# Kernel optimization log

Measured on AMD Instinct MI355X. Metric: run time of the kernel, lower is better.

Reference implementation:

```python
import jax, jax.numpy as jnp
import numpy as np

EMBED_DIM = 1024
EXPAND_RATIO = 128  # head_dim; n_heads = EMBED_DIM // EXPAND_RATIO = 8
B, N = 4, 2048


def setup_inputs() -> dict:
    key = jax.random.key(0)
    ks = jax.random.split(key, 6)
    std = 0.02
    d = EMBED_DIM
    return {
        "x": jax.random.normal(ks[0], (B, N, d), dtype=jnp.float32),
        "Wq": jax.random.normal(ks[1], (d, d), dtype=jnp.float32) * std,
        "Wk": jax.random.normal(ks[2], (d, d), dtype=jnp.float32) * std,
        "Wv": jax.random.normal(ks[3], (d, d), dtype=jnp.float32) * std,
        "Wo": jax.random.normal(ks[4], (d, d), dtype=jnp.float32) * std,
        "norm_w": jnp.ones((d,), dtype=jnp.float32),
    }


def _rmsnorm(x, w, eps=1e-6):
    return x * jax.lax.rsqrt(jnp.mean(x * x, axis=-1, keepdims=True) + eps) * w


def _gla_scan(q, k, v, g):
    # q,k,v,g: [b, n, h, d]; state S: [b, h, d_k, d_v]
    b, n, h, d = q.shape
    qs, ks_, vs, gs = (jnp.moveaxis(t, 1, 0) for t in (q, k, v, g))  # [n,b,h,d]
    S0 = jnp.zeros((b, h, d, d), dtype=q.dtype)

    def step(S, inp):
        q_t, k_t, v_t, g_t = inp
        # S_t = diag(exp(g_t)) S_{t-1} + k_t^T v_t (gate on key dim)
        S = jnp.exp(g_t)[..., :, None] * S + k_t[..., :, None] * v_t[..., None, :]
        o_t = jnp.einsum('bhk,bhkv->bhv', q_t, S)
        return S, o_t

    _, outs = jax.lax.scan(step, S0, (qs, ks_, vs, gs))
    return jnp.moveaxis(outs, 0, 1)  # [b, n, h, d]


def reference(x, Wq, Wk, Wv, Wo, norm_w):
    b, n, D = x.shape
    hd = EXPAND_RATIO
    h = D // hd

    q = jax.nn.silu(x @ Wq.T)          # q_activation = silu
    f = jax.nn.sigmoid(x @ Wk.T)       # f = sigmoid(k_proj(x))
    log_f = jax.nn.log_sigmoid(f)      # faithful: logsigmoid applied to f (lower_bound=None path)
    k = 1.0 - f
    v = x @ Wv.T

    def split_heads(t):
        return t.reshape(b, n, h, hd)

    out = _gla_scan(split_heads(q), split_heads(k), split_heads(v), split_heads(log_f))
    out = out.reshape(b, n, D)
    out = _rmsnorm(out, norm_w)        # norm_pos='ogate', no output gate
    return out @ Wo.T
```

## Files before the change

### kernel.cpp

```cpp
#include <hip/hip_runtime.h>
#include <cstdint>
#include <cstddef>


typedef unsigned short u16;
using f32x4  = __attribute__((ext_vector_type(4))) float;
using bf16x8 = __attribute__((ext_vector_type(8))) short;

__device__ __forceinline__ float bf2f(u16 u) {
  union { unsigned int i; float f; } v; v.i = ((unsigned int)u) << 16; return v.f;
}
__device__ __forceinline__ u16 f2bf(float f) {
  union { float f; unsigned int i; } v; v.f = f;
  unsigned int r = v.i + 0x7fffu + ((v.i >> 16) & 1u);
  return (u16)(r >> 16);
}
__device__ __forceinline__ void async_load16(const void* g, void* l) {
  __builtin_amdgcn_global_load_lds(
      (const __attribute__((address_space(1))) unsigned int*)(uintptr_t)g,
      (__attribute__((address_space(3))) unsigned int*)(uintptr_t)l, 16, 0, 0);
}

__device__ __forceinline__ void gemm128_core(const u16* __restrict__ Ag, const u16* __restrict__ Bg,
                                             u16* smem, f32x4 (&acc)[4][4]) {
  const int tid = threadIdx.x;
  const int lane = tid & 63, wave = tid >> 6;
  const int wm = (wave & 1) * 64, wn = (wave >> 1) * 64;
  const int r = lane & 15, quad = lane >> 4;
  const int xk = r & 3;
  const u16* baseA = smem + (wm + r) * 32 + ((quad ^ xk) & 3) * 8;
  const u16* baseB = smem + 4096 + (wn + r) * 32 + ((quad ^ xk) & 3) * 8;
  const int soff = (tid >> 2) * 1024 + (((tid & 3) ^ ((tid >> 2) & 3)) * 8);
  u16* dA = smem + wave * 512;
  u16* dB = smem + 4096 + wave * 512;
#pragma unroll
  for (int it = 0; it < 2; ++it) {
    async_load16(Ag + it * 65536 + soff, dA + it * 2048);
    async_load16(Bg + it * 65536 + soff, dB + it * 2048);
  }
#pragma unroll 2
  for (int kt = 0; kt < 32; ++kt) {
    const int cb = (kt & 1) * 8192;
    __syncthreads();
    if (kt < 31) {
      const int nb = ((kt + 1) & 1) * 8192;
      const u16* As = Ag + (kt + 1) * 32 + soff;
      const u16* Bs = Bg + (kt + 1) * 32 + soff;
#pragma unroll
      for (int it = 0; it < 2; ++it) {
        async_load16(As + it * 65536, dA + nb + it * 2048);
        async_load16(Bs + it * 65536, dB + nb + it * 2048);
      }
    }
    bf16x8 af[4], bv[4];
#pragma unroll
    for (int i = 0; i < 4; ++i) af[i] = *(const bf16x8*)(baseA + cb + i * 512);
#pragma unroll
    for (int j = 0; j < 4; ++j) bv[j] = *(const bf16x8*)(baseB + cb + j * 512);
#pragma unroll
    for (int i = 0; i < 4; ++i)
#pragma unroll
      for (int j = 0; j < 4; ++j)
        acc[i][j] = __builtin_amdgcn_mfma_f32_16x16x32_bf16(af[i], bv[j], acc[i][j], 0, 0, 0);
  }
}

__global__ __launch_bounds__(256) void cast_f32_bf16(const float* __restrict__ src,
                                                     u16* __restrict__ dst, int n4) {
  int i = blockIdx.x * 256 + threadIdx.x;
  if (i >= n4) return;
  float4 v = ((const float4*)src)[i];
  unsigned int lo = (unsigned)f2bf(v.x) | ((unsigned)f2bf(v.y) << 16);
  unsigned int hi = (unsigned)f2bf(v.z) | ((unsigned)f2bf(v.w) << 16);
  ((uint2*)dst)[i] = make_uint2(lo, hi);
}

__global__ __launch_bounds__(256) void cast_w4(const float* __restrict__ w0, const float* __restrict__ w1,
                                               const float* __restrict__ w2, const float* __restrict__ w3,
                                               u16* __restrict__ d0, u16* __restrict__ d1,
                                               u16* __restrict__ d2, u16* __restrict__ d3) {
  const float* src = blockIdx.y == 0 ? w0 : (blockIdx.y == 1 ? w1 : (blockIdx.y == 2 ? w2 : w3));
  u16* dst = blockIdx.y == 0 ? d0 : (blockIdx.y == 1 ? d1 : (blockIdx.y == 2 ? d2 : d3));
  int i = blockIdx.x * 256 + threadIdx.x;
  float4 v = ((const float4*)src)[i];
  unsigned int lo = (unsigned)f2bf(v.x) | ((unsigned)f2bf(v.y) << 16);
  unsigned int hi = (unsigned)f2bf(v.z) | ((unsigned)f2bf(v.w) << 16);
  ((uint2*)dst)[i] = make_uint2(lo, hi);
}

__global__ __launch_bounds__(256) void hgru_gemm_qkv(
    const u16* __restrict__ Xb, const u16* __restrict__ Wqb, const u16* __restrict__ Wkb,
    const u16* __restrict__ Wvb, u16* __restrict__ Qb, u16* __restrict__ Kb,
    u16* __restrict__ Vb) {
  __shared__ alignas(16) u16 smem[16384];
  const int which = blockIdx.y >> 3, bn = blockIdx.y & 7;
  const u16* W = which == 0 ? Wqb : (which == 1 ? Wkb : Wvb);
  const u16* Ag = Xb + (size_t)blockIdx.x * 128 * 1024;
  const u16* Bg = W + (size_t)bn * 128 * 1024;
  f32x4 acc[4][4] = {};
  gemm128_core(Ag, Bg, smem, acc);
  const int tid = threadIdx.x, lane = tid & 63, wave = tid >> 6;
  const int wm = (wave & 1) * 64, wn = (wave >> 1) * 64;
  const int r = lane & 15, quad = lane >> 4;
#pragma unroll
  for (int i = 0; i < 4; ++i)
#pragma unroll
    for (int j = 0; j < 4; ++j)
#pragma unroll
      for (int reg = 0; reg < 4; ++reg) {
        int m = blockIdx.x * 128 + wm + i * 16 + quad * 4 + reg;
        int n = bn * 128 + wn + j * 16 + r;
        size_t off = (size_t)m * 1024 + n;
        float z = acc[i][j][reg];
        if (which == 0) {
          Qb[off] = f2bf(z / (1.f + __expf(-z)));
        } else if (which == 1) {
          float ek = __expf(-z);
          Kb[off] = f2bf(ek / (1.f + ek));
        } else {
          Vb[off] = f2bf(z);
        }
      }
}

__global__ __launch_bounds__(256) void hgru_scan(
    const u16* __restrict__ Qg, const u16* __restrict__ Kg, const u16* __restrict__ Vg,
    u16* __restrict__ O) {
  __shared__ alignas(16) char smem[59008];
  float* sb = (float*)(smem);
  u16* sU   = (u16*)(smem + 16512);
  u16* sKt  = (u16*)(smem + 33920);
  u16* sVt1 = (u16*)(smem + 44160);
  u16* sQ   = (u16*)(smem + 33920);
  u16* sK   = (u16*)(smem + 42624);
  u16* sAm  = (u16*)(smem + 51328);
  u16* sVt2 = (u16*)(smem + 53888);

  const int tid = threadIdx.x, blk = blockIdx.x;
  const int vh = blk & 1, c = (blk >> 1) & 63, bh = blk >> 7, h = bh & 7, bb_ = bh >> 3;
  const size_t rb = (size_t)(bb_ * 2048 + c * 32) * 1024 + h * 128;
  const bool haveP = (c > 0);
  const size_t rb1 = haveP ? rb - 32 * 1024 : rb;

  const int lane = tid & 63, wave = tid >> 6;
  const int r = lane & 15, quad = lane >> 4;
  const int ts = tid & 31;
  const int g8 = tid >> 5;

  uint4 Q2[2], K2[2], K1[2], V2, V1;
#pragma unroll
  for (int it = 0; it < 2; ++it) {
    Q2[it] = *(const uint4*)(Qg + rb  + (size_t)ts * 1024 + (it * 8 + g8) * 8);
    K2[it] = *(const uint4*)(Kg + rb  + (size_t)ts * 1024 + (it * 8 + g8) * 8);
    K1[it] = *(const uint4*)(Kg + rb1 + (size_t)ts * 1024 + (it * 8 + g8) * 8);
  }
  V2 = *(const uint4*)(Vg + rb  + (size_t)ts * 1024 + vh * 64 + g8 * 8);
  V1 = *(const uint4*)(Vg + rb1 + (size_t)ts * 1024 + vh * 64 + g8 * 8);

  f32x4 accU[2][4] = {};
  const int vm = (wave & 1) * 32, in = (wave >> 1) * 64;

  if (haveP) {
    { const int col = tid & 127, half = tid >> 7;
      float run = 0.f;
      const size_t gb = rb1 + (size_t)(half * 16) * 1024 + col;
#pragma unroll
      for (int t = 0; t < 16; ++t) {
        float kv = bf2f(Kg[gb + (size_t)t * 1024]);
        run -= __logf(1.f + __expf(-(1.f - kv)));
        sb[(half * 16 + t) * 129 + col] = run;
      } }
    __syncthreads();
    { if (tid >> 7) { const int col = tid & 127; float fix = sb[15 * 129 + col];
#pragma unroll
        for (int t = 16; t < 32; ++t) sb[t * 129 + col] += fix; } }
    __syncthreads();
#pragma unroll
    for (int it = 0; it < 2; ++it) {
      const int i8 = it * 8 + g8;
      const u16* kp = (const u16*)&K1[it];
#pragma unroll
      for (int e = 0; e < 8; ++e) {
        int i = i8 * 8 + e;
        float bs = sb[ts * 129 + i];
        float bC = sb[31 * 129 + i];
        sKt[i * 40 + ts] = f2bf(bf2f(kp[e]) * __expf(bC - bs));
      }
    }
    { const u16* vp = (const u16*)&V1;
#pragma unroll
      for (int e = 0; e < 8; ++e) sVt1[(g8 * 8 + e) * 40 + ts] = vp[e]; }
    __syncthreads();
#pragma unroll
    for (int mi = 0; mi < 2; ++mi) {
      bf16x8 af = *(const bf16x8*)(sVt1 + (vm + mi * 16 + r) * 40 + quad * 8);
#pragma unroll
      for (int nj = 0; nj < 4; ++nj) {
        bf16x8 bv = *(const bf16x8*)(sKt + (in + nj * 16 + r) * 40 + quad * 8);
        accU[mi][nj] = __builtin_amdgcn_mfma_f32_16x16x32_bf16(af, bv, accU[mi][nj], 0, 0, 0);
      }
    }
  }
  { const int col = tid & 127, half = tid >> 7;
    float run = 0.f;
    const size_t gb = rb + (size_t)(half * 16) * 1024 + col;
#pragma unroll
    for (int t = 0; t < 16; ++t) {
      float kv = bf2f(Kg[gb + (size_t)t * 1024]);
      run -= __logf(1.f + __expf(-(1.f - kv)));
      sb[(half * 16 + t) * 129 + col] = run;
    } }
  __syncthreads();
  { if (tid >> 7) { const int col = tid & 127; float fix = sb[15 * 129 + col];
#pragma unroll
      for (int t = 16; t < 32; ++t) sb[t * 129 + col] += fix; } }
  if (haveP) {
#pragma unroll
    for (int mi = 0; mi < 2; ++mi)
#pragma unroll
      for (int nj = 0; nj < 4; ++nj)
#pragma unroll
        for (int reg = 0; reg < 4; ++reg) {
          int vl = vm + mi * 16 + quad * 4 + reg;
          int i  = in + nj * 16 + r;
          sU[vl * 136 + i] = f2bf(accU[mi][nj][reg]);
        }
  }
  __syncthreads();
#pragma unroll
  for (int it = 0; it < 2; ++it) {
    const int i8 = it * 8 + g8;
    const u16* qp = (const u16*)&Q2[it];
    const u16* kp = (const u16*)&K2[it];
    u16 qo[8], ko[8];
#pragma unroll
    for (int e = 0; e < 8; ++e) {
      int i = i8 * 8 + e;
      float bt = sb[ts * 129 + i];
      qo[e] = f2bf(bf2f(qp[e]) * __expf(bt));
      ko[e] = f2bf(bf2f(kp[e]) * __expf(-bt));
    }
    *(uint4*)(sQ + ts * 136 + i8 * 8) = *(const uint4*)qo;
    *(uint4*)(sK + ts * 136 + i8 * 8) = *(const uint4*)ko;
  }
  { const u16* vp = (const u16*)&V2;
#pragma unroll
    for (int e = 0; e < 8; ++e) sVt2[(g8 * 8 + e) * 40 + ts] = vp[e]; }
  __syncthreads();
  { const int mi = wave & 1, nj = wave >> 1;
    f32x4 a1 = {0.f, 0.f, 0.f, 0.f};
#pragma unroll
    for (int ks = 0; ks < 4; ++ks) {
      bf16x8 af = *(const bf16x8*)(sQ + (mi * 16 + r) * 136 + ks * 32 + quad * 8);
      bf16x8 bk = *(const bf16x8*)(sK + (nj * 16 + r) * 136 + ks * 32 + quad * 8);
      a1 = __builtin_amdgcn_mfma_f32_16x16x32_bf16(af, bk, a1, 0, 0, 0);
    }
#pragma unroll
    for (int reg = 0; reg < 4; ++reg) {
      int t = mi * 16 + quad * 4 + reg, s = nj * 16 + r;
      sAm[t * 40 + s] = (s <= t) ? f2bf(a1[reg]) : (u16)0;
    } }
  __syncthreads();
  { const int mi = wave & 1, no = (wave >> 1) * 32;
    bf16x8 af0 = *(const bf16x8*)(sAm + (mi * 16 + r) * 40 + quad * 8);
    bf16x8 afq[4];
    if (haveP) {
#pragma unroll
      for (int ks = 0; ks < 4; ++ks)
        afq[ks] = *(const bf16x8*)(sQ + (mi * 16 + r) * 136 + ks * 32 + quad * 8);
    }
#pragma unroll
    for (int j = 0; j < 2; ++j) {
      f32x4 acc2 = {0.f, 0.f, 0.f, 0.f};
      bf16x8 bv0 = *(const bf16x8*)(sVt2 + (no + j * 16 + r) * 40 + quad * 8);
      acc2 = __builtin_amdgcn_mfma_f32_16x16x32_bf16(af0, bv0, acc2, 0, 0, 0);
      if (haveP) {
#pragma unroll
        for (int ks = 0; ks < 4; ++ks) {
          bf16x8 bs = *(const bf16x8*)(sU + (no + j * 16 + r) * 136 + ks * 32 + quad * 8);
          acc2 = __builtin_amdgcn_mfma_f32_16x16x32_bf16(afq[ks], bs, acc2, 0, 0, 0);
        }
      }
#pragma unroll
      for (int reg = 0; reg < 4; ++reg) {
        int t = mi * 16 + quad * 4 + reg;
        int vg = vh * 64 + no + j * 16 + r;
        O[rb + (size_t)t * 1024 + vg] = f2bf(acc2[reg]);
      }
    } }
}

__global__ __launch_bounds__(256) void hgru_rmsnorm(const u16* __restrict__ O,
                                                    const float* __restrict__ w,
                                                    u16* __restrict__ On) {
  __shared__ float sred[4];
  const int row = blockIdx.x, tid = threadIdx.x;
  const size_t base = (size_t)row * 1024;
  float vals[4];
  float ss = 0.f;
#pragma unroll
  for (int k = 0; k < 4; ++k) {
    float v = bf2f(O[base + k * 256 + tid]);
    vals[k] = v;
    ss += v * v;
  }
#pragma unroll
  for (int m = 32; m >= 1; m >>= 1) ss += __shfl_xor(ss, m);
  if ((tid & 63) == 0) sred[tid >> 6] = ss;
  __syncthreads();
  float tot = sred[0] + sred[1] + sred[2] + sred[3];
  float scale = rsqrtf(tot * (1.f / 1024.f) + 1e-6f);
#pragma unroll
  for (int k = 0; k < 4; ++k)
    On[base + k * 256 + tid] = f2bf(vals[k] * scale * w[k * 256 + tid]);
}

__global__ __launch_bounds__(256) void hgru_gemm_out(const u16* __restrict__ Ab,
                                                     const u16* __restrict__ Wob,
                                                     float* __restrict__ out) {
  __shared__ alignas(16) u16 smem[16384];
  const u16* Ag = Ab + (size_t)blockIdx.x * 128 * 1024;
  const u16* Bg = Wob + (size_t)blockIdx.y * 128 * 1024;
  f32x4 acc[4][4] = {};
  gemm128_core(Ag, Bg, smem, acc);
  const int tid = threadIdx.x, lane = tid & 63, wave = tid >> 6;
  const int wm = (wave & 1) * 64, wn = (wave >> 1) * 64;
  const int r = lane & 15, quad = lane >> 4;
#pragma unroll
  for (int i = 0; i < 4; ++i)
#pragma unroll
    for (int j = 0; j < 4; ++j)
#pragma unroll
      for (int reg = 0; reg < 4; ++reg) {
        int m = blockIdx.x * 128 + wm + i * 16 + quad * 4 + reg;
        int n = blockIdx.y * 128 + wn + j * 16 + r;
        out[(size_t)m * 1024 + n] = acc[i][j][reg];
      }
}

extern "C" void kernel_launch(void* const* d_in, const int* in_sizes, int n_in,
                              void* d_out, int out_size, void* d_ws, size_t ws_size,
                              hipStream_t stream) {
  const float* x  = (const float*)d_in[0];
  const float* Wq = (const float*)d_in[1];
  const float* Wk = (const float*)d_in[2];
  const float* Wv = (const float*)d_in[3];
  const float* Wo = (const float*)d_in[4];
  const float* nw = (const float*)d_in[5];
  float* out = (float*)d_out;
  char* ws = (char*)d_ws;

  u16* Xb   = (u16*)(ws + 0);
  u16* Wqb  = (u16*)(ws + 16777216);
  u16* Wkb  = (u16*)(ws + 18874368);
  u16* Wvb  = (u16*)(ws + 20971520);
  u16* Wob  = (u16*)(ws + 23068672);
  u16* Qb   = (u16*)(ws + 25165824);
  u16* Kb   = (u16*)(ws + 41943040);
  u16* Vb   = (u16*)(ws + 58720256);
  u16* Obf  = (u16*)(ws + 75497472);
  u16* On   = Xb;

  cast_f32_bf16<<<8192, 256, 0, stream>>>(x, Xb, 2097152);
  dim3 gw(1024, 4);
  cast_w4<<<gw, 256, 0, stream>>>(Wq, Wk, Wv, Wo, Wqb, Wkb, Wvb, Wob);

  dim3 gq(64, 24);
  hgru_gemm_qkv<<<gq, 256, 0, stream>>>(Xb, Wqb, Wkb, Wvb, Qb, Kb, Vb);
  hgru_scan<<<4096, 256, 0, stream>>>(Qb, Kb, Vb, Obf);
  hgru_rmsnorm<<<8192, 256, 0, stream>>>(Obf, nw, On);
  dim3 go(64, 8);
  hgru_gemm_out<<<go, 256, 0, stream>>>(On, Wob, out);
}
```

Before: 255.8 us.

## Fold RMSNorm into output GEMM epilogue and shrink scan shared memory

The norm weight is now folded into Wo during the weight cast. The RMSNorm kernel becomes a row sum-of-squares pass that writes only one scale per row, and that scale is applied in the output GEMM epilogue. This removes the full normalized-activation write and reread. The scan kernel also reorders its work so sU can alias the sb buffer, which reduces shared memory from about 59 KB to 42 KB to allow more resident blocks. The trade-off is an extra barrier, and the unnormalized bf16 output now feeds the GEMM directly, which changes rounding slightly.

```diff
diff --git a/kernel.cpp b/kernel.cpp
--- a/kernel.cpp
+++ b/kernel.cpp
@@ -77,12 +77,17 @@
 
 __global__ __launch_bounds__(256) void cast_w4(const float* __restrict__ w0, const float* __restrict__ w1,
                                                const float* __restrict__ w2, const float* __restrict__ w3,
+                                               const float* __restrict__ nw,
                                                u16* __restrict__ d0, u16* __restrict__ d1,
                                                u16* __restrict__ d2, u16* __restrict__ d3) {
   const float* src = blockIdx.y == 0 ? w0 : (blockIdx.y == 1 ? w1 : (blockIdx.y == 2 ? w2 : w3));
   u16* dst = blockIdx.y == 0 ? d0 : (blockIdx.y == 1 ? d1 : (blockIdx.y == 2 ? d2 : d3));
   int i = blockIdx.x * 256 + threadIdx.x;
   float4 v = ((const float4*)src)[i];
+  if (blockIdx.y == 3) {
+    float4 wv = ((const float4*)nw)[i & 255];
+    v.x *= wv.x; v.y *= wv.y; v.z *= wv.z; v.w *= wv.w;
+  }
   unsigned int lo = (unsigned)f2bf(v.x) | ((unsigned)f2bf(v.y) << 16);
   unsigned int hi = (unsigned)f2bf(v.z) | ((unsigned)f2bf(v.w) << 16);
   ((uint2*)dst)[i] = make_uint2(lo, hi);
@@ -126,15 +131,15 @@
 __global__ __launch_bounds__(256) void hgru_scan(
     const u16* __restrict__ Qg, const u16* __restrict__ Kg, const u16* __restrict__ Vg,
     u16* __restrict__ O) {
-  __shared__ alignas(16) char smem[59008];
-  float* sb = (float*)(smem);
-  u16* sU   = (u16*)(smem + 16512);
-  u16* sKt  = (u16*)(smem + 33920);
-  u16* sVt1 = (u16*)(smem + 44160);
-  u16* sQ   = (u16*)(smem + 33920);
-  u16* sK   = (u16*)(smem + 42624);
-  u16* sAm  = (u16*)(smem + 51328);
-  u16* sVt2 = (u16*)(smem + 53888);
+  __shared__ alignas(16) char smem[42496];
+  float* sb  = (float*)(smem);
+  u16* sU    = (u16*)(smem);
+  u16* sKt   = (u16*)(smem + 17408);
+  u16* sVt1  = (u16*)(smem + 27648);
+  u16* sQ    = (u16*)(smem + 17408);
+  u16* sK    = (u16*)(smem + 26112);
+  u16* sVt2  = (u16*)(smem + 34816);
+  u16* sAm   = (u16*)(smem + 39936);
 
   const int tid = threadIdx.x, blk = blockIdx.x;
   const int vh = blk & 1, c = (blk >> 1) & 63, bh = blk >> 7, h = bh & 7, bb_ = bh >> 3;
@@ -214,6 +219,40 @@
   { if (tid >> 7) { const int col = tid & 127; float fix = sb[15 * 129 + col];
 #pragma unroll
       for (int t = 16; t < 32; ++t) sb[t * 129 + col] += fix; } }
+  __syncthreads();
+#pragma unroll
+  for (int it = 0; it < 2; ++it) {
+    const int i8 = it * 8 + g8;
+    const u16* qp = (const u16*)&Q2[it];
+    const u16* kp = (const u16*)&K2[it];
+    u16 qo[8], ko[8];
+#pragma unroll
+    for (int e = 0; e < 8; ++e) {
+      int i = i8 * 8 + e;
+      float bt = sb[ts * 129 + i];
+      qo[e] = f2bf(bf2f(qp[e]) * __expf(bt));
+      ko[e] = f2bf(bf2f(kp[e]) * __expf(-bt));
+    }
+    *(uint4*)(sQ + ts * 136 + i8 * 8) = *(const uint4*)qo;
+    *(uint4*)(sK + ts * 136 + i8 * 8) = *(const uint4*)ko;
+  }
+  { const u16* vp = (const u16*)&V2;
+#pragma unroll
+    for (int e = 0; e < 8; ++e) sVt2[(g8 * 8 + e) * 40 + ts] = vp[e]; }
+  __syncthreads();
+  { const int mi = wave & 1, nj = wave >> 1;
+    f32x4 a1 = {0.f, 0.f, 0.f, 0.f};
+#pragma unroll
+    for (int ks = 0; ks < 4; ++ks) {
+      bf16x8 af = *(const bf16x8*)(sQ + (mi * 16 + r) * 136 + ks * 32 + quad * 8);
+      bf16x8 bk = *(const bf16x8*)(sK + (nj * 16 + r) * 136 + ks * 32 + quad * 8);
+      a1 = __builtin_amdgcn_mfma_f32_16x16x32_bf16(af, bk, a1, 0, 0, 0);
+    }
+#pragma unroll
+    for (int reg = 0; reg < 4; ++reg) {
+      int t = mi * 16 + quad * 4 + reg, s = nj * 16 + r;
+      sAm[t * 40 + s] = (s <= t) ? f2bf(a1[reg]) : (u16)0;
+    } }
   if (haveP) {
 #pragma unroll
     for (int mi = 0; mi < 2; ++mi)
@@ -227,40 +266,6 @@
         }
   }
   __syncthreads();
-#pragma unroll
-  for (int it = 0; it < 2; ++it) {
-    const int i8 = it * 8 + g8;
-    const u16* qp = (const u16*)&Q2[it];
-    const u16* kp = (const u16*)&K2[it];
-    u16 qo[8], ko[8];
-#pragma unroll
-    for (int e = 0; e < 8; ++e) {
-      int i = i8 * 8 + e;
-      float bt = sb[ts * 129 + i];
-      qo[e] = f2bf(bf2f(qp[e]) * __expf(bt));
-      ko[e] = f2bf(bf2f(kp[e]) * __expf(-bt));
-    }
-    *(uint4*)(sQ + ts * 136 + i8 * 8) = *(const uint4*)qo;
-    *(uint4*)(sK + ts * 136 + i8 * 8) = *(const uint4*)ko;
-  }
-  { const u16* vp = (const u16*)&V2;
-#pragma unroll
-    for (int e = 0; e < 8; ++e) sVt2[(g8 * 8 + e) * 40 + ts] = vp[e]; }
-  __syncthreads();
-  { const int mi = wave & 1, nj = wave >> 1;
-    f32x4 a1 = {0.f, 0.f, 0.f, 0.f};
-#pragma unroll
-    for (int ks = 0; ks < 4; ++ks) {
-      bf16x8 af = *(const bf16x8*)(sQ + (mi * 16 + r) * 136 + ks * 32 + quad * 8);
-      bf16x8 bk = *(const bf16x8*)(sK + (nj * 16 + r) * 136 + ks * 32 + quad * 8);
-      a1 = __builtin_amdgcn_mfma_f32_16x16x32_bf16(af, bk, a1, 0, 0, 0);
-    }
-#pragma unroll
-    for (int reg = 0; reg < 4; ++reg) {
-      int t = mi * 16 + quad * 4 + reg, s = nj * 16 + r;
-      sAm[t * 40 + s] = (s <= t) ? f2bf(a1[reg]) : (u16)0;
-    } }
-  __syncthreads();
   { const int mi = wave & 1, no = (wave >> 1) * 32;
     bf16x8 af0 = *(const bf16x8*)(sAm + (mi * 16 + r) * 40 + quad * 8);
     bf16x8 afq[4];
@@ -290,33 +295,34 @@
     } }
 }
 
-__global__ __launch_bounds__(256) void hgru_rmsnorm(const u16* __restrict__ O,
-                                                    const float* __restrict__ w,
-                                                    u16* __restrict__ On) {
-  __shared__ float sred[4];
-  const int row = blockIdx.x, tid = threadIdx.x;
-  const size_t base = (size_t)row * 1024;
-  float vals[4];
+__global__ __launch_bounds__(256) void hgru_sumsq(const u16* __restrict__ O,
+                                                  float* __restrict__ s) {
+  const int row = blockIdx.x * 4 + (threadIdx.x >> 6);
+  const int lane = threadIdx.x & 63;
+  const u16* p = O + (size_t)row * 1024 + lane * 16;
+  uint4 a = *(const uint4*)p;
+  uint4 b = *(const uint4*)(p + 8);
   float ss = 0.f;
-#pragma unroll
-  for (int k = 0; k < 4; ++k) {
-    float v = bf2f(O[base + k * 256 + tid]);
-    vals[k] = v;
-    ss += v * v;
+  const unsigned int* w = (const unsigned int*)&a;
+#pragma unroll
+  for (int e = 0; e < 4; ++e) {
+    float lo = bf2f((u16)(w[e] & 0xffff)), hi = bf2f((u16)(w[e] >> 16));
+    ss += lo * lo + hi * hi;
+  }
+  const unsigned int* w2 = (const unsigned int*)&b;
+#pragma unroll
+  for (int e = 0; e < 4; ++e) {
+    float lo = bf2f((u16)(w2[e] & 0xffff)), hi = bf2f((u16)(w2[e] >> 16));
+    ss += lo * lo + hi * hi;
   }
 #pragma unroll
   for (int m = 32; m >= 1; m >>= 1) ss += __shfl_xor(ss, m);
-  if ((tid & 63) == 0) sred[tid >> 6] = ss;
-  __syncthreads();
-  float tot = sred[0] + sred[1] + sred[2] + sred[3];
-  float scale = rsqrtf(tot * (1.f / 1024.f) + 1e-6f);
-#pragma unroll
-  for (int k = 0; k < 4; ++k)
-    On[base + k * 256 + tid] = f2bf(vals[k] * scale * w[k * 256 + tid]);
+  if (lane == 0) s[row] = rsqrtf(ss * (1.f / 1024.f) + 1e-6f);
 }
 
 __global__ __launch_bounds__(256) void hgru_gemm_out(const u16* __restrict__ Ab,
                                                      const u16* __restrict__ Wob,
+                                                     const float* __restrict__ s,
                                                      float* __restrict__ out) {
   __shared__ alignas(16) u16 smem[16384];
   const u16* Ag = Ab + (size_t)blockIdx.x * 128 * 1024;
@@ -329,13 +335,15 @@
 #pragma unroll
   for (int i = 0; i < 4; ++i)
 #pragma unroll
-    for (int j = 0; j < 4; ++j)
-#pragma unroll
-      for (int reg = 0; reg < 4; ++reg) {
-        int m = blockIdx.x * 128 + wm + i * 16 + quad * 4 + reg;
+    for (int reg = 0; reg < 4; ++reg) {
+      int m = blockIdx.x * 128 + wm + i * 16 + quad * 4 + reg;
+      float sm = s[m];
+#pragma unroll
+      for (int j = 0; j < 4; ++j) {
         int n = blockIdx.y * 128 + wn + j * 16 + r;
-        out[(size_t)m * 1024 + n] = acc[i][j][reg];
-      }
+        out[(size_t)m * 1024 + n] = acc[i][j][reg] * sm;
+      }
+    }
 }
 
 extern "C" void kernel_launch(void* const* d_in, const int* in_sizes, int n_in,
@@ -359,16 +367,16 @@
   u16* Kb   = (u16*)(ws + 41943040);
   u16* Vb   = (u16*)(ws + 58720256);
   u16* Obf  = (u16*)(ws + 75497472);
-  u16* On   = Xb;
+  float* Sv = (float*)(ws + 92274688);
 
   cast_f32_bf16<<<8192, 256, 0, stream>>>(x, Xb, 2097152);
   dim3 gw(1024, 4);
-  cast_w4<<<gw, 256, 0, stream>>>(Wq, Wk, Wv, Wo, Wqb, Wkb, Wvb, Wob);
+  cast_w4<<<gw, 256, 0, stream>>>(Wq, Wk, Wv, Wo, nw, Wqb, Wkb, Wvb, Wob);
 
   dim3 gq(64, 24);
   hgru_gemm_qkv<<<gq, 256, 0, stream>>>(Xb, Wqb, Wkb, Wvb, Qb, Kb, Vb);
   hgru_scan<<<4096, 256, 0, stream>>>(Qb, Kb, Vb, Obf);
-  hgru_rmsnorm<<<8192, 256, 0, stream>>>(Obf, nw, On);
+  hgru_sumsq<<<2048, 256, 0, stream>>>(Obf, Sv);
   dim3 go(64, 8);
-  hgru_gemm_out<<<go, 256, 0, stream>>>(On, Wob, out);
-}
+  hgru_gemm_out<<<go, 256, 0, stream>>>(Obf, Wob, Sv, out);
+}
```

Result: faster. 239.5 us (-6.4%).
